# Optimization experiments

Measured on AMD Instinct MI355X. Metric: run time of the kernel, lower is better.

Reference implementation:

```python
import jax, jax.numpy as jnp
import numpy as np

B = 1024          # batch
IN_FEATURES = 20000
N_GROUP = 64
G_IN = 512        # indices gathered per group
H1 = 256          # first Linear out dim per group
GROUP_SIZE = 128  # second Linear out dim per group


def setup_inputs() -> dict:
    key = jax.random.key(0)
    k_x, k_idx, k_w1, k_b1, k_w2, k_b2 = jax.random.split(key, 6)
    x = jax.random.normal(k_x, (B, IN_FEATURES), dtype=jnp.float32)
    idx = jax.random.randint(k_idx, (N_GROUP, G_IN), 0, IN_FEATURES, dtype=jnp.int64)
    # Stacked per-group Linear weights (uniform group shapes allow batching).
    s1 = 1.0 / np.sqrt(G_IN)
    s2 = 1.0 / np.sqrt(H1)
    W1 = jax.random.uniform(k_w1, (N_GROUP, G_IN, H1), jnp.float32, -s1, s1)
    b1 = jax.random.uniform(k_b1, (N_GROUP, H1), jnp.float32, -s1, s1)
    W2 = jax.random.uniform(k_w2, (N_GROUP, H1, GROUP_SIZE), jnp.float32, -s2, s2)
    b2 = jax.random.uniform(k_b2, (N_GROUP, GROUP_SIZE), jnp.float32, -s2, s2)
    return {"x": x, "idx": idx, "W1": W1, "b1": b1, "W2": W2, "b2": b2}


def reference(x, idx, W1, b1, W2, b2):
    # Per-group gather of input columns: [B, n_group, G_IN]
    g = x[:, idx]
    # Two bare Linears per group (no activation, matching the source Sequential).
    h = jnp.einsum('bgi,gio->bgo', g, W1) + b1          # [B, n_group, H1]
    o = jnp.einsum('bgh,gho->bgo', h, W2) + b2          # [B, n_group, GROUP_SIZE]
    # Concat groups along feature dim -> [B, n_group*GROUP_SIZE]
    return o.reshape(o.shape[0], -1)
```

## Files before the change

### kernel.cpp

```cpp
#include <hip/hip_runtime.h>
#include <hip/hip_bf16.h>
#include <stdint.h>


typedef __attribute__((ext_vector_type(4))) float f32x4;
typedef __attribute__((ext_vector_type(8))) __bf16 bf16x8;
typedef __attribute__((ext_vector_type(8))) uint16_t u16x8;

__device__ __forceinline__ uint16_t f2bf(float f) {
    uint32_t u = __float_as_uint(f);
    u += 0x7FFFu + ((u >> 16) & 1u);
    return (uint16_t)(u >> 16);
}

__device__ __forceinline__ uint64_t pack4bf(f32x4 v) {
    return (uint64_t)f2bf(v[0]) | ((uint64_t)f2bf(v[1]) << 16)
         | ((uint64_t)f2bf(v[2]) << 32) | ((uint64_t)f2bf(v[3]) << 48);
}

__global__ __launch_bounds__(512) void k_prep(const float* __restrict__ x,
                                              const int* __restrict__ idx,
                                              const float* __restrict__ W1,
                                              const float* __restrict__ b1,
                                              const float* __restrict__ W2,
                                              const float* __restrict__ b2,
                                              uint16_t* __restrict__ Wc,
                                              float* __restrict__ bias2,
                                              uint32_t* __restrict__ G32) {
    __shared__ __align__(16) uint64_t smem8[5000];
    const int bid = blockIdx.x;
    const int t = threadIdx.x;

    if (bid < 256) {
        uint16_t* As = (uint16_t*)smem8;
        uint16_t* Bs = As + 5120;
        const int g = bid >> 2, mt = bid & 3;
        const int wid = t >> 6, l = t & 63;
        const int wm = wid >> 1, wn = wid & 1;
        const int q = l >> 4, lm = l & 15;
        const float* W1g = W1 + ((size_t)g * 512 + (size_t)mt * 128) * 256;
        const float* W2g = W2 + (size_t)g * 256 * 128;
        f32x4 acc[2][4];
        #pragma unroll
        for (int mi = 0; mi < 2; ++mi)
            #pragma unroll
            for (int ni = 0; ni < 4; ++ni) {
                f32x4 z = {0.f, 0.f, 0.f, 0.f};
                acc[mi][ni] = z;
            }
        for (int kt = 0; kt < 8; ++kt) {
            __syncthreads();
            #pragma unroll
            for (int i = 0; i < 2; ++i) {
                int f4 = t + i * 512;
                int m = f4 >> 3, c4 = f4 & 7;
                f32x4 v = *(const f32x4*)(W1g + (size_t)m * 256 + kt * 32 + c4 * 4);
                *(uint64_t*)&As[m * 40 + c4 * 4] = pack4bf(v);
            }
            #pragma unroll
            for (int i = 0; i < 2; ++i) {
                int f4 = t + i * 512;
                int h = f4 >> 5, n4 = f4 & 31;
                f32x4 v = *(const f32x4*)(W2g + (size_t)(kt * 32 + h) * 128 + n4 * 4);
                *(uint64_t*)&Bs[h * 132 + n4 * 4] = pack4bf(v);
            }
            __syncthreads();
            bf16x8 a[2];
            #pragma unroll
            for (int mi = 0; mi < 2; ++mi)
                a[mi] = *(const bf16x8*)&As[(wm * 32 + mi * 16 + lm) * 40 + q * 8];
            #pragma unroll
            for (int ni = 0; ni < 4; ++ni) {
                int n = wn * 64 + ni * 16 + lm;
                u16x8 bu;
                #pragma unroll
                for (int j = 0; j < 8; ++j) bu[j] = Bs[(q * 8 + j) * 132 + n];
                bf16x8 bv = __builtin_bit_cast(bf16x8, bu);
                #pragma unroll
                for (int mi = 0; mi < 2; ++mi)
                    acc[mi][ni] = __builtin_amdgcn_mfma_f32_16x16x32_bf16(a[mi], bv, acc[mi][ni], 0, 0, 0);
            }
        }
        uint16_t* Wcg = Wc + (size_t)g * 128 * 512;
        #pragma unroll
        for (int mi = 0; mi < 2; ++mi) {
            int k0 = mt * 128 + wm * 32 + mi * 16 + q * 4;
            #pragma unroll
            for (int ni = 0; ni < 4; ++ni) {
                int n = wn * 64 + ni * 16 + lm;
                f32x4 c = acc[mi][ni];
                *(uint64_t*)&Wcg[(size_t)n * 512 + k0] = pack4bf(c);
            }
        }
    } else if (bid < 320) {
        if (t < 128) {
            const int g = bid - 256, n = t;
            const float* w = W2 + (size_t)g * 256 * 128 + n;
            const float* bb = b1 + g * 256;
            float s = b2[g * 128 + n];
            for (int h = 0; h < 256; ++h) s += bb[h] * w[(size_t)h * 128];
            bias2[g * 128 + n] = s;
        }
    } else {
        uint16_t* sh = (uint16_t*)smem8;
        const int b = bid - 320;
        const f32x4* xr = (const f32x4*)(x + (size_t)b * 20000);
        for (int i = t; i < 5000; i += 512) {
            f32x4 v = xr[i];
            *(uint64_t*)&sh[i * 4] = pack4bf(v);
        }
        __syncthreads();
        const int4* idx4 = (const int4*)idx;
        const size_t bbase = (size_t)b * 256;
        #pragma unroll 4
        for (int i = t; i < 8192; i += 512) {
            int4 iv = idx4[i];
            uint32_t w0 = (uint32_t)sh[iv.x] | ((uint32_t)sh[iv.y] << 16);
            uint32_t w1 = (uint32_t)sh[iv.z] | ((uint32_t)sh[iv.w] << 16);
            int g = i >> 7, kq = i & 127;
            uint2 p; p.x = w0; p.y = w1;
            *(uint2*)&G32[(size_t)g * 262144 + bbase + kq * 2] = p;
        }
    }
}

__global__ __launch_bounds__(256) void k_gemm(const uint16_t* __restrict__ G,
                                              const uint16_t* __restrict__ Wc,
                                              const float* __restrict__ bias2,
                                              float* __restrict__ out) {
    __shared__ uint16_t sh[16384];
    uint16_t* As = sh;
    uint16_t* Bs = sh + 8192;
    const int g = blockIdx.x >> 3, mt = blockIdx.x & 7;
    const int t = threadIdx.x;
    const int wid = t >> 6, l = t & 63;
    const int wm = wid >> 1, wn = wid & 1;
    const int q = l >> 4, lm = l & 15;
    const int lrow = l >> 3;
    const int lcolsw = ((l & 7) ^ lrow) * 8;
    const uint16_t* Ga = G + (size_t)g * 524288 + (size_t)mt * 128 * 512;
    const uint16_t* Wa = Wc + (size_t)g * 65536;

    f32x4 acc[4][4];
    #pragma unroll
    for (int mi = 0; mi < 4; ++mi)
        #pragma unroll
        for (int ni = 0; ni < 4; ++ni) {
            f32x4 z = {0.f, 0.f, 0.f, 0.f};
            acc[mi][ni] = z;
        }

    for (int kt = 0; kt < 8; ++kt) {
        __syncthreads();
        #pragma unroll
        for (int r = 0; r < 4; ++r) {
            const int rowbase = wid * 8 + r * 32;
            const uint16_t* sA = Ga + (size_t)(rowbase + lrow) * 512 + kt * 64 + lcolsw;
            const uint16_t* sB = Wa + (size_t)(rowbase + lrow) * 512 + kt * 64 + lcolsw;
            __builtin_amdgcn_global_load_lds(
                (const __attribute__((address_space(1))) void*)sA,
                (__attribute__((address_space(3))) void*)(As + rowbase * 64), 16, 0, 0);
            __builtin_amdgcn_global_load_lds(
                (const __attribute__((address_space(1))) void*)sB,
                (__attribute__((address_space(3))) void*)(Bs + rowbase * 64), 16, 0, 0);
        }
        __syncthreads();
        #pragma unroll
        for (int kk = 0; kk < 2; ++kk) {
            bf16x8 a[4], b[4];
            #pragma unroll
            for (int mi = 0; mi < 4; ++mi) {
                int row = wm * 64 + mi * 16 + lm;
                int off = row * 64 + ((kk * 32 + q * 8) ^ ((lm & 7) * 8));
                a[mi] = *(const bf16x8*)&As[off];
            }
            #pragma unroll
            for (int ni = 0; ni < 4; ++ni) {
                int row = wn * 64 + ni * 16 + lm;
                int off = row * 64 + ((kk * 32 + q * 8) ^ ((lm & 7) * 8));
                b[ni] = *(const bf16x8*)&Bs[off];
            }
            #pragma unroll
            for (int mi = 0; mi < 4; ++mi)
                #pragma unroll
                for (int ni = 0; ni < 4; ++ni)
                    acc[mi][ni] = __builtin_amdgcn_mfma_f32_16x16x32_bf16(a[mi], b[ni], acc[mi][ni], 0, 0, 0);
        }
    }
    float bn[4];
    #pragma unroll
    for (int ni = 0; ni < 4; ++ni) bn[ni] = bias2[g * 128 + wn * 64 + ni * 16 + lm];
    #pragma unroll
    for (int mi = 0; mi < 4; ++mi)
        #pragma unroll
        for (int ni = 0; ni < 4; ++ni) {
            int col = g * 128 + wn * 64 + ni * 16 + lm;
            #pragma unroll
            for (int r = 0; r < 4; ++r) {
                int brow = mt * 128 + wm * 64 + mi * 16 + q * 4 + r;
                out[(size_t)brow * 8192 + col] = acc[mi][ni][r] + bn[ni];
            }
        }
}

extern "C" void kernel_launch(void* const* d_in, const int* in_sizes, int n_in,
                              void* d_out, int out_size, void* d_ws, size_t ws_size,
                              hipStream_t stream) {
    (void)in_sizes; (void)n_in; (void)out_size; (void)ws_size;
    const float* x   = (const float*)d_in[0];
    const int*   idx = (const int*)d_in[1];
    const float* W1  = (const float*)d_in[2];
    const float* b1  = (const float*)d_in[3];
    const float* W2  = (const float*)d_in[4];
    const float* b2  = (const float*)d_in[5];
    float* out = (float*)d_out;

    uint16_t* G     = (uint16_t*)d_ws;
    uint16_t* Wc    = (uint16_t*)((char*)d_ws + (size_t)(64 << 20));
    float*    bias2 = (float*)   ((char*)d_ws + (size_t)(72 << 20));

    k_prep<<<1344, 512, 0, stream>>>(x, idx, W1, b1, W2, b2, Wc, bias2, (uint32_t*)G);
    k_gemm<<<512,  256, 0, stream>>>(G, Wc, bias2, out);
}
```

Before: 70.30 us.

## Process two batch rows per prep block with prefetch overlap; remap gemm blocks

The prep kernel now uses 1024-thread blocks. Each gather block handles two batch rows and loads the second row's x into registers while it gathers the first from LDS, and the index loads are software-prefetched. The weight-fold GEMM is redistributed over 16 waves, each holding a smaller accumulator tile. The gemm kernel's block index is remapped so that blocks sharing a group's weights are spread across CUs (XCD-aware). In exchange, the larger blocks raise register pressure and reduce block-level parallelism.

```diff
diff --git a/kernel.cpp b/kernel.cpp
--- a/kernel.cpp
+++ b/kernel.cpp
@@ -18,49 +18,78 @@
          | ((uint64_t)f2bf(v[2]) << 32) | ((uint64_t)f2bf(v[3]) << 48);
 }
 
-__global__ __launch_bounds__(512) void k_prep(const float* __restrict__ x,
-                                              const int* __restrict__ idx,
-                                              const float* __restrict__ W1,
-                                              const float* __restrict__ b1,
-                                              const float* __restrict__ W2,
-                                              const float* __restrict__ b2,
-                                              uint16_t* __restrict__ Wc,
-                                              float* __restrict__ bias2,
-                                              uint32_t* __restrict__ G32) {
-    __shared__ __align__(16) uint64_t smem8[5000];
+__device__ __forceinline__ void row_load(const float* __restrict__ xrow, int t, f32x4 r[5]) {
+    #pragma unroll
+    for (int i = 0; i < 5; ++i) {
+        int si = t + i * 1024;
+        si = si < 4999 ? si : 4999;
+        r[i] = *(const f32x4*)(xrow + (size_t)si * 4);
+    }
+}
+
+__device__ __forceinline__ void row_write(uint16_t* sh, int t, const f32x4 r[5]) {
+    #pragma unroll
+    for (int i = 0; i < 5; ++i) {
+        int si = t + i * 1024;
+        if (si < 5000) *(uint64_t*)&sh[si * 4] = pack4bf(r[i]);
+    }
+}
+
+__device__ __forceinline__ void row_gather(const uint16_t* sh, const int4* __restrict__ idx4,
+                                           int t, int b, uint32_t* __restrict__ G32) {
+    int4 nv = idx4[t];
+    #pragma unroll
+    for (int it = 0; it < 8; ++it) {
+        int4 cv = nv;
+        if (it < 7) nv = idx4[t + (it + 1) * 1024];
+        int j = t + it * 1024;
+        uint32_t w0 = (uint32_t)sh[cv.x] | ((uint32_t)sh[cv.y] << 16);
+        uint32_t w1 = (uint32_t)sh[cv.z] | ((uint32_t)sh[cv.w] << 16);
+        int g = j >> 7, kd = j & 127;
+        uint2 p; p.x = w0; p.y = w1;
+        *(uint2*)&G32[(size_t)g * 262144 + (size_t)b * 256 + kd * 2] = p;
+    }
+}
+
+__global__ __launch_bounds__(1024, 8) void k_prep(const float* __restrict__ x,
+                                                  const int* __restrict__ idx,
+                                                  const float* __restrict__ W1,
+                                                  const float* __restrict__ b1,
+                                                  const float* __restrict__ W2,
+                                                  const float* __restrict__ b2,
+                                                  uint16_t* __restrict__ Wc,
+                                                  float* __restrict__ bias2,
+                                                  uint32_t* __restrict__ G32) {
+    __shared__ __align__(16) uint8_t smem[40960];
     const int bid = blockIdx.x;
     const int t = threadIdx.x;
 
     if (bid < 256) {
-        uint16_t* As = (uint16_t*)smem8;
+        uint16_t* As = (uint16_t*)smem;
         uint16_t* Bs = As + 5120;
         const int g = bid >> 2, mt = bid & 3;
         const int wid = t >> 6, l = t & 63;
-        const int wm = wid >> 1, wn = wid & 1;
+        const int wm = wid >> 2, wn = wid & 3;
         const int q = l >> 4, lm = l & 15;
         const float* W1g = W1 + ((size_t)g * 512 + (size_t)mt * 128) * 256;
         const float* W2g = W2 + (size_t)g * 256 * 128;
-        f32x4 acc[2][4];
+        f32x4 acc[2][2];
         #pragma unroll
         for (int mi = 0; mi < 2; ++mi)
             #pragma unroll
-            for (int ni = 0; ni < 4; ++ni) {
+            for (int ni = 0; ni < 2; ++ni) {
                 f32x4 z = {0.f, 0.f, 0.f, 0.f};
                 acc[mi][ni] = z;
             }
         for (int kt = 0; kt < 8; ++kt) {
             __syncthreads();
-            #pragma unroll
-            for (int i = 0; i < 2; ++i) {
-                int f4 = t + i * 512;
-                int m = f4 >> 3, c4 = f4 & 7;
+            {
+                int m = t >> 3, c4 = t & 7;
                 f32x4 v = *(const f32x4*)(W1g + (size_t)m * 256 + kt * 32 + c4 * 4);
                 *(uint64_t*)&As[m * 40 + c4 * 4] = pack4bf(v);
             }
-            #pragma unroll
-            for (int i = 0; i < 2; ++i) {
-                int f4 = t + i * 512;
-                int h = f4 >> 5, n4 = f4 & 31;
+            {
+                int h = t >> 5, n4 = t & 31;
                 f32x4 v = *(const f32x4*)(W2g + (size_t)(kt * 32 + h) * 128 + n4 * 4);
                 *(uint64_t*)&Bs[h * 132 + n4 * 4] = pack4bf(v);
             }
@@ -70,8 +99,8 @@
             for (int mi = 0; mi < 2; ++mi)
                 a[mi] = *(const bf16x8*)&As[(wm * 32 + mi * 16 + lm) * 40 + q * 8];
             #pragma unroll
-            for (int ni = 0; ni < 4; ++ni) {
-                int n = wn * 64 + ni * 16 + lm;
+            for (int ni = 0; ni < 2; ++ni) {
+                int n = wn * 32 + ni * 16 + lm;
                 u16x8 bu;
                 #pragma unroll
                 for (int j = 0; j < 8; ++j) bu[j] = Bs[(q * 8 + j) * 132 + n];
@@ -86,10 +115,9 @@
         for (int mi = 0; mi < 2; ++mi) {
             int k0 = mt * 128 + wm * 32 + mi * 16 + q * 4;
             #pragma unroll
-            for (int ni = 0; ni < 4; ++ni) {
-                int n = wn * 64 + ni * 16 + lm;
-                f32x4 c = acc[mi][ni];
-                *(uint64_t*)&Wcg[(size_t)n * 512 + k0] = pack4bf(c);
+            for (int ni = 0; ni < 2; ++ni) {
+                int n = wn * 32 + ni * 16 + lm;
+                *(uint64_t*)&Wcg[(size_t)n * 512 + k0] = pack4bf(acc[mi][ni]);
             }
         }
     } else if (bid < 320) {
@@ -102,25 +130,21 @@
             bias2[g * 128 + n] = s;
         }
     } else {
-        uint16_t* sh = (uint16_t*)smem8;
-        const int b = bid - 320;
-        const f32x4* xr = (const f32x4*)(x + (size_t)b * 20000);
-        for (int i = t; i < 5000; i += 512) {
-            f32x4 v = xr[i];
-            *(uint64_t*)&sh[i * 4] = pack4bf(v);
-        }
-        __syncthreads();
+        uint16_t* sh = (uint16_t*)smem;
+        const int gb = bid - 320;
+        const int b0 = gb * 2, b1r = b0 + 1;
         const int4* idx4 = (const int4*)idx;
-        const size_t bbase = (size_t)b * 256;
-        #pragma unroll 4
-        for (int i = t; i < 8192; i += 512) {
-            int4 iv = idx4[i];
-            uint32_t w0 = (uint32_t)sh[iv.x] | ((uint32_t)sh[iv.y] << 16);
-            uint32_t w1 = (uint32_t)sh[iv.z] | ((uint32_t)sh[iv.w] << 16);
-            int g = i >> 7, kq = i & 127;
-            uint2 p; p.x = w0; p.y = w1;
-            *(uint2*)&G32[(size_t)g * 262144 + bbase + kq * 2] = p;
-        }
+        f32x4 r[5];
+        row_load(x + (size_t)b0 * 20000, t, r);
+        row_write(sh, t, r);
+        __syncthreads();
+        row_load(x + (size_t)b1r * 20000, t, r);
+        __builtin_amdgcn_sched_barrier(0);
+        row_gather(sh, idx4, t, b0, G32);
+        __syncthreads();
+        row_write(sh, t, r);
+        __syncthreads();
+        row_gather(sh, idx4, t, b1r, G32);
     }
 }
 
@@ -131,7 +155,8 @@
     __shared__ uint16_t sh[16384];
     uint16_t* As = sh;
     uint16_t* Bs = sh + 8192;
-    const int g = blockIdx.x >> 3, mt = blockIdx.x & 7;
+    const int wg = (blockIdx.x & 7) * 64 + (blockIdx.x >> 3);
+    const int g = wg >> 3, mt = wg & 7;
     const int t = threadIdx.x;
     const int wid = t >> 6, l = t & 63;
     const int wm = wid >> 1, wn = wid & 1;
@@ -219,6 +244,6 @@
     uint16_t* Wc    = (uint16_t*)((char*)d_ws + (size_t)(64 << 20));
     float*    bias2 = (float*)   ((char*)d_ws + (size_t)(72 << 20));
 
-    k_prep<<<1344, 512, 0, stream>>>(x, idx, W1, b1, W2, b2, Wc, bias2, (uint32_t*)G);
+    k_prep<<<832, 1024, 0, stream>>>(x, idx, W1, b1, W2, b2, Wc, bias2, (uint32_t*)G);
     k_gemm<<<512,  256, 0, stream>>>(G, Wc, bias2, out);
 }
```

New measurement: 69.29 us. No clear change (-1.4%).
